# Kernel optimization log

Measured on AMD Instinct MI355X. Metric: run time of the kernel, lower is better.

## Reference

```python
import jax, jax.numpy as jnp
import numpy as np

H = 8          # query heads
KVH = 4        # key/value heads
D = 256        # head_dim
HID = 2304     # hidden_size
B = 1
S = 4096
SW = 2048      # sliding window
THETA = 10000.0
SCALE = 256 ** -0.5          # query_pre_attn_scalar ** -0.5
SOFTCAP = 50.0
NEG = -1e9


def setup_inputs() -> dict:
    key = jax.random.key(0)
    ks = jax.random.split(key, 6)
    hidden_states = jax.random.normal(ks[0], (B, S, HID), jnp.float32)
    Wq = jax.random.normal(ks[1], (H * D, HID), jnp.float32) * 0.02
    Wk = jax.random.normal(ks[2], (KVH * D, HID), jnp.float32) * 0.02
    Wv = jax.random.normal(ks[3], (KVH * D, HID), jnp.float32) * 0.02
    Wo = jax.random.normal(ks[4], (HID, H * D), jnp.float32) * 0.02
    # causal + sliding-window additive mask: allowed iff 0 <= i-j < SW
    i = jnp.arange(S)[:, None]
    j = jnp.arange(S)[None, :]
    ok = (i >= j) & ((i - j) < SW)
    attention_mask = jnp.where(ok, 0.0, NEG).astype(jnp.float32)[None, None]
    position_ids = jnp.arange(S, dtype=jnp.int32)[None, :]
    return {"hidden_states": hidden_states, "attention_mask": attention_mask,
            "Wq": Wq, "Wk": Wk, "Wv": Wv, "Wo": Wo, "position_ids": position_ids}


def _rope(q, k, position_ids):
    # cos/sin: [B, 1, S, D]
    pos = position_ids.astype(jnp.float32)                      # [B, S]
    inv_freq = 1.0 / (THETA ** (jnp.arange(0, D, 2, dtype=jnp.float32) / D))
    freqs = pos[:, :, None] * inv_freq[None, None, :]           # [B, S, D/2]
    emb = jnp.concatenate([freqs, freqs], axis=-1)              # [B, S, D]
    cos = jnp.cos(emb)[:, None]
    sin = jnp.sin(emb)[:, None]
    rot = lambda x: jnp.concatenate([-x[..., D // 2:], x[..., :D // 2]], axis=-1)
    return q * cos + rot(q) * sin, k * cos + rot(k) * sin


def reference(hidden_states, attention_mask, Wq, Wk, Wv, Wo, position_ids):
    b, s, _ = hidden_states.shape
    q = (hidden_states @ Wq.T).reshape(b, s, H, D).transpose(0, 2, 1, 3)    # [B,H,S,D]
    k = (hidden_states @ Wk.T).reshape(b, s, KVH, D).transpose(0, 2, 1, 3)  # [B,KVH,S,D]
    v = (hidden_states @ Wv.T).reshape(b, s, KVH, D).transpose(0, 2, 1, 3)
    q, k = _rope(q, k, position_ids)
    rep = H // KVH
    k = jnp.repeat(k, rep, axis=1)
    v = jnp.repeat(v, rep, axis=1)
    scores = jnp.einsum('bhqd,bhkd->bhqk', q * SCALE, k)
    scores = jnp.tanh(scores / SOFTCAP) * SOFTCAP + attention_mask
    probs = jax.nn.softmax(scores.astype(jnp.float32), axis=-1).astype(q.dtype)
    out = jnp.einsum('bhqk,bhkd->bhqd', probs, v)
    out = out.transpose(0, 2, 1, 3).reshape(b, s, H * D)
    return out @ Wo.T
```

## Files before the change

### kernel.cpp

```cpp
#include <hip/hip_runtime.h>
#include <hip/hip_bf16.h>
#include <math.h>

#define S 4096
#define HQ 8
#define NKVH 4
#define D 256
#define HID 2304
#define SW 2048
#define QDIM 2048
#define KVDIM 1024
#define QKVDIM 4096
#define SCALE 0.0625f
#define SOFTCAP 50.0f

typedef __attribute__((ext_vector_type(4))) float f32x4;
typedef __attribute__((ext_vector_type(8))) short short8;

__device__ __forceinline__ float bf2f(unsigned v) { return __uint_as_float(v << 16); }
__device__ __forceinline__ unsigned f2bf(float f) {
    unsigned u = __float_as_uint(f);
    return (u + 0x7fffu + ((u >> 16) & 1u)) >> 16;
}

__device__ __forceinline__ void store_c(float* p, float v) { *p = v; }
__device__ __forceinline__ void store_c(unsigned short* p, float v) { *p = (unsigned short)f2bf(v); }

__device__ __forceinline__ void glls16(const void* g, void* l) {
    __builtin_amdgcn_global_load_lds(
        (const __attribute__((address_space(1))) unsigned int*)g,
        (__attribute__((address_space(3))) unsigned int*)l, 16, 0, 0);
}

__global__ __launch_bounds__(256) void cvt_bf16(const float* __restrict__ in,
                                                unsigned short* __restrict__ out)
{
    int i = blockIdx.x * 256 + threadIdx.x;
    float4 v = ((const float4*)in)[i];
    uint2 o;
    o.x = f2bf(v.x) | (f2bf(v.y) << 16);
    o.y = f2bf(v.z) | (f2bf(v.w) << 16);
    ((uint2*)out)[i] = o;
}

template <typename TC>
__global__ __launch_bounds__(256) void bf16_gemm_bt(const unsigned short* __restrict__ A,
                                                    const unsigned short* __restrict__ B,
                                                    TC* __restrict__ C,
                                                    int M, int N, int K)
{
    __shared__ unsigned short As[2][16 * 512];
    __shared__ unsigned short Bs[2][16 * 512];
    const int t = threadIdx.x;

    const int nbx = gridDim.x;
    const int nwg = nbx * gridDim.y;
    int flat = blockIdx.y * nbx + blockIdx.x;
    const int q8 = nwg >> 3, r8 = nwg & 7;
    const int xcd = flat & 7, orig = flat >> 3;
    const int wg = (xcd < r8 ? xcd * (q8 + 1) : r8 * (q8 + 1) + (xcd - r8) * q8) + orig;
    const int band = wg / (8 * nbx);
    const int rem  = wg - band * 8 * nbx;
    const int m0 = (band * 8 + (rem & 7)) * 128;
    const int n0 = (rem >> 3) * 128;

    const int w = t >> 6, lid = t & 63, n16 = lid & 15, quad = lid >> 4;
    const int wm = (w >> 1) * 64, wn = (w & 1) * 64;

    f32x4 acc[4][4] = {};

    auto stage = [&](int buf, int k0) {
        #pragma unroll
        for (int it = 0; it < 4; ++it) {
            int f  = it * 4 + w;
            int fm = f >> 1, fk = f & 1;
            const size_t goff = (size_t)(fm * 16 + n16) * K + k0 + fk * 32 + quad * 8;
            glls16(A + (size_t)m0 * K + goff, &As[buf][f * 512]);
            glls16(B + (size_t)n0 * K + goff, &Bs[buf][f * 512]);
        }
    };

    const int nk = K / 64;
    stage(0, 0);
    int cur = 0;
    for (int kk = 0; kk < nk; ++kk) {
        asm volatile("s_waitcnt vmcnt(0)" ::: "memory");
        __syncthreads();
        if (kk + 1 < nk) stage(cur ^ 1, (kk + 1) * 64);
        #pragma unroll
        for (int ks = 0; ks < 2; ++ks) {
            short8 af[4], bfr[4];
            #pragma unroll
            for (int x = 0; x < 4; ++x) {
                af[x]  = *(const short8*)(&As[cur][(((wm >> 4) + x) * 2 + ks) * 512 + lid * 8]);
                bfr[x] = *(const short8*)(&Bs[cur][(((wn >> 4) + x) * 2 + ks) * 512 + lid * 8]);
            }
            __builtin_amdgcn_s_setprio(1);
            #pragma unroll
            for (int i = 0; i < 4; ++i)
                #pragma unroll
                for (int j = 0; j < 4; ++j)
                    acc[i][j] = __builtin_amdgcn_mfma_f32_16x16x32_bf16(af[i], bfr[j], acc[i][j], 0, 0, 0);
            __builtin_amdgcn_s_setprio(0);
        }
        cur ^= 1;
    }

    #pragma unroll
    for (int i = 0; i < 4; ++i) {
        #pragma unroll
        for (int j = 0; j < 4; ++j) {
            int rbase = m0 + wm + i * 16 + quad * 4;
            int col   = n0 + wn + j * 16 + n16;
            #pragma unroll
            for (int rg = 0; rg < 4; ++rg)
                store_c(C + (size_t)(rbase + rg) * N + col, acc[i][j][rg]);
        }
    }
}

__global__ __launch_bounds__(256) void rope_kernel(const unsigned short* __restrict__ QKV,
                                                   unsigned short* __restrict__ Qb,
                                                   unsigned short* __restrict__ Kb,
                                                   const int* __restrict__ pos_ids)
{
    int id   = blockIdx.x * 256 + threadIdx.x;
    int d    = id & 127;
    int rest = id >> 7;
    int hh   = rest % 12;
    int i    = rest / 12;
    float pos = (float)pos_ids[i];
    float inv = __expf((float)d * (-9.210340371976184f / 128.0f));
    float ang = pos * inv;
    float sn, cs;
    sincosf(ang, &sn, &cs);
    if (hh < HQ) {
        const unsigned short* p = QKV + (size_t)i * QKVDIM + hh * D + d;
        float x0 = bf2f(p[0]), x1 = bf2f(p[128]);
        unsigned short* q = Qb + (size_t)i * QDIM + hh * D + d;
        q[0]   = (unsigned short)f2bf((x0 * cs - x1 * sn) * SCALE);
        q[128] = (unsigned short)f2bf((x1 * cs + x0 * sn) * SCALE);
    } else {
        const unsigned short* p = QKV + (size_t)i * QKVDIM + QDIM + (hh - HQ) * D + d;
        float x0 = bf2f(p[0]), x1 = bf2f(p[128]);
        unsigned short* k = Kb + (size_t)i * KVDIM + (hh - HQ) * D + d;
        k[0]   = (unsigned short)f2bf(x0 * cs - x1 * sn);
        k[128] = (unsigned short)f2bf(x1 * cs + x0 * sn);
    }
}

__global__ __launch_bounds__(256) void transpose_v(const unsigned short* __restrict__ QKV,
                                                   unsigned short* __restrict__ Vt)
{
    __shared__ float tile[64][65];
    const int s0 = blockIdx.x * 64, d0 = blockIdx.y * 64;
    const int t = threadIdx.x;
    #pragma unroll
    for (int it = 0; it < 4; ++it) {
        int flat = it * 256 + t;
        int r  = flat >> 4;
        int c4 = (flat & 15) * 4;
        uint2 v = *(const uint2*)(QKV + (size_t)(s0 + r) * QKVDIM + (QDIM + KVDIM) + d0 + c4);
        tile[r][c4 + 0] = bf2f(v.x & 0xffffu); tile[r][c4 + 1] = bf2f(v.x >> 16);
        tile[r][c4 + 2] = bf2f(v.y & 0xffffu); tile[r][c4 + 3] = bf2f(v.y >> 16);
    }
    __syncthreads();
    #pragma unroll
    for (int it = 0; it < 4; ++it) {
        int flat = it * 256 + t;
        int dr  = flat >> 4;
        int sc4 = (flat & 15) * 4;
        uint2 o;
        o.x = f2bf(tile[sc4 + 0][dr]) | (f2bf(tile[sc4 + 1][dr]) << 16);
        o.y = f2bf(tile[sc4 + 2][dr]) | (f2bf(tile[sc4 + 3][dr]) << 16);
        *(uint2*)(Vt + (size_t)(d0 + dr) * S + s0 + sc4) = o;
    }
}

__global__ __launch_bounds__(256, 2) void attn_kernel(const unsigned short* __restrict__ Qb,
                                                      const unsigned short* __restrict__ Kb,
                                                      const unsigned short* __restrict__ Vt,
                                                      unsigned short* __restrict__ O)
{
    __shared__ unsigned short Ks[2][32 * 256];
    __shared__ unsigned short Vs[2][256 * 32];
    __shared__ unsigned short Ps[4 * 512];
    const int t = threadIdx.x;
    const int bid = blockIdx.x;
    const int b2 = bid & 255;
    const int h = b2 & 7, kvh = h >> 1;
    const int u = b2 >> 3;
    const int g = (bid < 256) ? u : 63 - u;
    const int i0 = g * 64;
    const int w = t >> 6, lid = t & 63, n16 = lid & 15, quad = lid >> 4;
    const int qbase = i0 + w * 16;
    unsigned short* Pw = Ps + w * 512;

    auto stage = [&](int buf, int j0) {
        #pragma unroll
        for (int it = 0; it < 4; ++it) {
            int f = it * 4 + w;
            int nt = f >> 3, ks = f & 7;
            glls16(Kb + (size_t)(j0 + nt * 16 + n16) * KVDIM + kvh * D + ks * 32 + quad * 8,
                   &Ks[buf][f * 512]);
        }
        #pragma unroll
        for (int it = 0; it < 4; ++it) {
            int f = it * 4 + w;
            glls16(Vt + (size_t)(kvh * D + f * 16 + n16) * S + j0 + quad * 8,
                   &Vs[buf][f * 512]);
        }
    };

    short8 qf[8];
    #pragma unroll
    for (int ks = 0; ks < 8; ++ks)
        qf[ks] = *(const short8*)(Qb + (size_t)(qbase + n16) * QDIM + h * D + ks * 32 + quad * 8);

    float lacc[4] = {0.f, 0.f, 0.f, 0.f};
    f32x4 Oacc[16] = {};

    const int jt_min = (i0 >= SW) ? ((i0 - (SW - 1)) >> 5) : 0;
    const int jt_max = (i0 + 63) >> 5;

    stage(0, jt_min * 32);
    int cur = 0;

    for (int jt = jt_min; jt <= jt_max; ++jt) {
        const int j0 = jt * 32;
        asm volatile("s_waitcnt vmcnt(0)" ::: "memory");
        __syncthreads();
        if (jt < jt_max) stage(cur ^ 1, (jt + 1) * 32);

        f32x4 sc[2] = {};
        __builtin_amdgcn_s_setprio(1);
        #pragma unroll
        for (int ks = 0; ks < 8; ++ks) {
            #pragma unroll
            for (int nt = 0; nt < 2; ++nt) {
                short8 kf = *(const short8*)(&Ks[cur][(nt * 8 + ks) * 512 + lid * 8]);
                sc[nt] = __builtin_amdgcn_mfma_f32_16x16x32_bf16(qf[ks], kf, sc[nt], 0, 0, 0);
            }
        }
        __builtin_amdgcn_s_setprio(0);

        #pragma unroll
        for (int nt = 0; nt < 2; ++nt) {
            int j = j0 + nt * 16 + n16;
            #pragma unroll
            for (int rg = 0; rg < 4; ++rg) {
                int iq = qbase + quad * 4 + rg;
                float e = __expf(sc[nt][rg] * (2.0f / SOFTCAP));
                float p = __expf(-100.0f * __builtin_amdgcn_rcpf(e + 1.0f));
                bool ok = (j <= iq) && (iq - j < SW);
                p = ok ? p : 0.0f;
                lacc[rg] += p;
                Pw[(quad * 4 + rg + 16 * (nt * 2 + (n16 >> 3))) * 8 + (n16 & 7)]
                    = (unsigned short)f2bf(p);
            }
        }

        asm volatile("s_waitcnt lgkmcnt(0)" ::: "memory");

        short8 pf = *(const short8*)(Pw + lid * 8);
        __builtin_amdgcn_s_setprio(1);
        #pragma unroll
        for (int dt = 0; dt < 16; ++dt) {
            short8 vf = *(const short8*)(&Vs[cur][dt * 512 + lid * 8]);
            Oacc[dt] = __builtin_amdgcn_mfma_f32_16x16x32_bf16(pf, vf, Oacc[dt], 0, 0, 0);
        }
        __builtin_amdgcn_s_setprio(0);
        cur ^= 1;
    }

    float linv[4];
    #pragma unroll
    for (int rg = 0; rg < 4; ++rg) {
        float rs = lacc[rg];
        rs += __shfl_xor(rs, 1); rs += __shfl_xor(rs, 2);
        rs += __shfl_xor(rs, 4); rs += __shfl_xor(rs, 8);
        linv[rg] = 1.0f / rs;
    }
    #pragma unroll
    for (int dt = 0; dt < 16; ++dt) {
        int col = h * D + dt * 16 + n16;
        #pragma unroll
        for (int rg = 0; rg < 4; ++rg) {
            int row = qbase + quad * 4 + rg;
            O[(size_t)row * QDIM + col] = (unsigned short)f2bf(Oacc[dt][rg] * linv[rg]);
        }
    }
}

extern "C" void kernel_launch(void* const* d_in, const int* in_sizes, int n_in,
                              void* d_out, int out_size, void* d_ws, size_t ws_size,
                              hipStream_t stream) {
    const float* hidden = (const float*)d_in[0];
    const float* Wq = (const float*)d_in[2];
    const float* Wk = (const float*)d_in[3];
    const float* Wv = (const float*)d_in[4];
    const float* Wo = (const float*)d_in[5];
    const int* pos = (const int*)d_in[6];
    float* out = (float*)d_out;

    char* ws = (char*)d_ws;
    unsigned short* Hb   = (unsigned short*)(ws);
    unsigned short* Qb   = (unsigned short*)(ws);
    unsigned short* Wqkv = (unsigned short*)(ws + (size_t)(18 << 20));
    unsigned short* QKVf = (unsigned short*)(ws + (size_t)(37 << 20));
    unsigned short* Oa   = (unsigned short*)(ws + (size_t)(37 << 20));
    unsigned short* Kb   = (unsigned short*)(ws + (size_t)(69 << 20));
    unsigned short* Vt   = (unsigned short*)(ws + (size_t)(77 << 20));

    cvt_bf16<<<(S * HID) / 1024, 256, 0, stream>>>(hidden, Hb);
    cvt_bf16<<<(QDIM * HID) / 1024, 256, 0, stream>>>(Wq, Wqkv);
    cvt_bf16<<<(KVDIM * HID) / 1024, 256, 0, stream>>>(Wk, Wqkv + (size_t)QDIM * HID);
    cvt_bf16<<<(KVDIM * HID) / 1024, 256, 0, stream>>>(Wv, Wqkv + (size_t)(QDIM + KVDIM) * HID);

    bf16_gemm_bt<unsigned short><<<dim3(QKVDIM / 128, S / 128), 256, 0, stream>>>(
        Hb, Wqkv, QKVf, S, QKVDIM, HID);

    rope_kernel<<<(S * 12 * 128) / 256, 256, 0, stream>>>(QKVf, Qb, Kb, pos);
    transpose_v<<<dim3(S / 64, KVDIM / 64), 256, 0, stream>>>(QKVf, Vt);

    attn_kernel<<<512, 256, 0, stream>>>(Qb, Kb, Vt, Oa);

    cvt_bf16<<<(HID * QDIM) / 1024, 256, 0, stream>>>(Wo, Wqkv);
    bf16_gemm_bt<float><<<dim3(HID / 128, S / 128), 256, 0, stream>>>(Oa, Wqkv, out, S, HID, QDIM);
}
```

Before: 591.6 us.

## Add 256x256-tile 8-phase pipelined bf16 GEMM for QKV projection

Replaces the 128x128-tile QKV projection GEMM with a new 512-thread kernel that uses 256x256 output tiles and an 8-phase software pipeline. Each phase issues a quarter of the next k-slice's global-to-LDS loads while the MFMAs for the current sub-tile run. Blocks are remapped across XCD-like groups for locality. The aim is more data reuse per tile and better overlap of memory traffic with compute, at the cost of higher register and LDS pressure. The grid also shrinks to 256 blocks, which may leave some CUs underused.

```diff
diff --git a/kernel.cpp b/kernel.cpp
--- a/kernel.cpp
+++ b/kernel.cpp
@@ -115,6 +115,112 @@
             #pragma unroll
             for (int rg = 0; rg < 4; ++rg)
                 store_c(C + (size_t)(rbase + rg) * N + col, acc[i][j][rg]);
+        }
+    }
+}
+
+__global__ __launch_bounds__(512, 2) void bf16_gemm_8ph(const unsigned short* __restrict__ A,
+                                                        const unsigned short* __restrict__ B,
+                                                        unsigned short* __restrict__ C,
+                                                        int M, int N, int K)
+{
+    __shared__ unsigned short As[2][32 * 512];
+    __shared__ unsigned short Bs[2][32 * 512];
+    const int t = threadIdx.x;
+    const int w = t >> 6, lid = t & 63, n16 = lid & 15, quad = lid >> 4;
+
+    const int flat = blockIdx.x;
+    const int wg = (flat & 7) * 32 + (flat >> 3);
+    const int m0 = (wg >> 4) * 256, n0 = (wg & 15) * 256;
+
+    const int wmf = (w >> 2) * 8;
+    const int wnf = (w & 3) * 4;
+    const int fnw = (w >> 1) * 4 + (w & 1);
+
+    f32x4 acc[8][4] = {};
+
+    auto stageA = [&](int buf, int k0, int fm) {
+        glls16(A + (size_t)(m0 + fm * 16 + n16) * K + k0 + quad * 8,
+               &As[buf][(fm * 2 + 0) * 512]);
+        glls16(A + (size_t)(m0 + fm * 16 + n16) * K + k0 + 32 + quad * 8,
+               &As[buf][(fm * 2 + 1) * 512]);
+    };
+    auto stageB = [&](int buf, int k0, int fn) {
+        glls16(B + (size_t)(n0 + fn * 16 + n16) * K + k0 + quad * 8,
+               &Bs[buf][(fn * 2 + 0) * 512]);
+        glls16(B + (size_t)(n0 + fn * 16 + n16) * K + k0 + 32 + quad * 8,
+               &Bs[buf][(fn * 2 + 1) * 512]);
+    };
+    auto sAm0 = [&](int buf, int k0){ stageA(buf, k0, (w & 3) + (w >> 2) * 8); };
+    auto sAm1 = [&](int buf, int k0){ stageA(buf, k0, 4 + (w & 3) + (w >> 2) * 8); };
+    auto sBn0 = [&](int buf, int k0){ stageB(buf, k0, fnw); };
+    auto sBn1 = [&](int buf, int k0){ stageB(buf, k0, fnw + 2); };
+
+#define GPHASE(mh, nh, buf, STAGE, WAITSTR)                                          \
+    {                                                                                \
+        short8 afr[4][2], bfr[2][2];                                                 \
+        _Pragma("unroll") for (int i = 0; i < 4; ++i)                                \
+            _Pragma("unroll") for (int ks = 0; ks < 2; ++ks)                         \
+                afr[i][ks] = *(const short8*)(&As[buf][((wmf + (mh)*4 + i)*2 + ks)*512 + lid*8]); \
+        _Pragma("unroll") for (int j = 0; j < 2; ++j)                                \
+            _Pragma("unroll") for (int ks = 0; ks < 2; ++ks)                         \
+                bfr[j][ks] = *(const short8*)(&Bs[buf][((wnf + (nh)*2 + j)*2 + ks)*512 + lid*8]); \
+        STAGE;                                                                       \
+        __builtin_amdgcn_s_barrier();                                                \
+        asm volatile("s_waitcnt lgkmcnt(0)" ::: "memory");                           \
+        __builtin_amdgcn_sched_barrier(0);                                           \
+        __builtin_amdgcn_s_setprio(1);                                               \
+        _Pragma("unroll") for (int i = 0; i < 4; ++i)                                \
+            _Pragma("unroll") for (int j = 0; j < 2; ++j)                            \
+                _Pragma("unroll") for (int ks = 0; ks < 2; ++ks)                     \
+                    acc[(mh)*4 + i][(nh)*2 + j] = __builtin_amdgcn_mfma_f32_16x16x32_bf16( \
+                        afr[i][ks], bfr[j][ks], acc[(mh)*4 + i][(nh)*2 + j], 0, 0, 0); \
+        __builtin_amdgcn_s_setprio(0);                                               \
+        asm volatile(WAITSTR ::: "memory");                                          \
+        __builtin_amdgcn_s_barrier();                                                \
+    }
+
+    const int nk = K / 64;
+    const int niter = nk / 2;
+
+    sAm0(0, 0); sBn0(0, 0); sAm1(0, 0); sBn1(0, 0);
+    sAm0(1, 64); sBn0(1, 64);
+    asm volatile("s_waitcnt vmcnt(4)" ::: "memory");
+    __builtin_amdgcn_s_barrier();
+
+    for (int I = 0; I < niter - 1; ++I) {
+        const int kc = I * 128;
+        GPHASE(0, 0, 0, sAm1(1, kc + 64);,  "")
+        GPHASE(0, 1, 0, sBn1(1, kc + 64);,  "")
+        GPHASE(1, 0, 0, sAm0(0, kc + 128);, "")
+        GPHASE(1, 1, 0, sBn0(0, kc + 128);, "s_waitcnt vmcnt(4)")
+        GPHASE(0, 0, 1, sAm1(0, kc + 128);, "")
+        GPHASE(0, 1, 1, sBn1(0, kc + 128);, "")
+        GPHASE(1, 0, 1, sAm0(1, kc + 192);, "")
+        GPHASE(1, 1, 1, sBn0(1, kc + 192);, "s_waitcnt vmcnt(4)")
+    }
+    {
+        const int kc = (niter - 1) * 128;
+        GPHASE(0, 0, 0, sAm1(1, kc + 64);, "")
+        GPHASE(0, 1, 0, sBn1(1, kc + 64);, "")
+        GPHASE(1, 0, 0, {};,               "")
+        GPHASE(1, 1, 0, {};,               "s_waitcnt vmcnt(0)")
+        GPHASE(0, 0, 1, {};,               "")
+        GPHASE(0, 1, 1, {};,               "")
+        GPHASE(1, 0, 1, {};,               "")
+        GPHASE(1, 1, 1, {};,               "")
+    }
+#undef GPHASE
+
+    #pragma unroll
+    for (int mi = 0; mi < 8; ++mi) {
+        #pragma unroll
+        for (int nj = 0; nj < 4; ++nj) {
+            int rbase = m0 + (w >> 2) * 128 + mi * 16 + quad * 4;
+            int col   = n0 + (w & 3) * 64 + nj * 16 + n16;
+            #pragma unroll
+            for (int rg = 0; rg < 4; ++rg)
+                store_c(C + (size_t)(rbase + rg) * N + col, acc[mi][nj][rg]);
         }
     }
 }
@@ -317,8 +423,7 @@
     cvt_bf16<<<(KVDIM * HID) / 1024, 256, 0, stream>>>(Wk, Wqkv + (size_t)QDIM * HID);
     cvt_bf16<<<(KVDIM * HID) / 1024, 256, 0, stream>>>(Wv, Wqkv + (size_t)(QDIM + KVDIM) * HID);
 
-    bf16_gemm_bt<unsigned short><<<dim3(QKVDIM / 128, S / 128), 256, 0, stream>>>(
-        Hb, Wqkv, QKVf, S, QKVDIM, HID);
+    bf16_gemm_8ph<<<256, 512, 0, stream>>>(Hb, Wqkv, QKVf, S, QKVDIM, HID);
 
     rope_kernel<<<(S * 12 * 128) / 256, 256, 0, stream>>>(QKVf, Qb, Kb, pos);
     transpose_v<<<dim3(S / 64, KVDIM / 64), 256, 0, stream>>>(QKVf, Vt);
```

Measured after the change: 568.7 us. 3.9% less time.
